# Kernel optimization log

Measured on AMD Instinct MI355X. Metric: run time of the kernel, lower is better.

Reference implementation:

```python
import jax, jax.numpy as jnp
import numpy as np
import math

D_MODEL = 1024
NUM_NEURONS = 2048
LUT_SIZE = 4096
TWO_PI = 2.0 * math.pi


def lut_sin_cos(theta, sin_table, cos_table):
    # Interpolated periodic table lookup over [0, 2*pi)
    n = sin_table.shape[0]
    pos = (theta / TWO_PI) * n
    pos = jnp.mod(pos, n)
    i0 = jnp.floor(pos).astype(jnp.int32)
    frac = pos - i0.astype(theta.dtype)
    i1 = jnp.mod(i0 + 1, n)
    s = sin_table[i0] * (1.0 - frac) + sin_table[i1] * frac
    c = cos_table[i0] * (1.0 - frac) + cos_table[i1] * frac
    return s, c


def setup_inputs() -> dict:
    key = jax.random.key(0)
    ks = jax.random.split(key, 10)
    B = 64
    x_real = jax.random.normal(ks[0], (B, D_MODEL), jnp.float32)
    x_imag = jax.random.normal(ks[1], (B, D_MODEL), jnp.float32)
    t = jax.random.uniform(ks[2], (B,), jnp.float32)
    # xavier_uniform with gain=0.5 for linear weights
    def xavier(k, shape, gain):
        fan_out, fan_in = shape
        a = gain * math.sqrt(6.0 / (fan_in + fan_out))
        return jax.random.uniform(k, shape, jnp.float32, -a, a)
    ic_w = xavier(ks[3], (D_MODEL, 2 * D_MODEL), 0.5)
    ic_b = jnp.zeros((D_MODEL,), jnp.float32)
    W = jax.random.normal(ks[4], (NUM_NEURONS, D_MODEL), jnp.float32) * 0.02
    Bp = jnp.zeros((NUM_NEURONS, D_MODEL), jnp.float32)
    attn_cos = jnp.ones((NUM_NEURONS, D_MODEL), jnp.float32)
    attn_sin = jnp.ones((NUM_NEURONS, D_MODEL), jnp.float32)
    wr = xavier(ks[5], (D_MODEL, NUM_NEURONS), 0.5)
    wi = xavier(ks[6], (D_MODEL, NUM_NEURONS), 0.5)
    grid = jnp.arange(LUT_SIZE, dtype=jnp.float32) * (TWO_PI / LUT_SIZE)
    sin_table = jnp.sin(grid)
    cos_table = jnp.cos(grid)
    return {"x_real": x_real, "x_imag": x_imag, "t": t,
            "ic_w": ic_w, "ic_b": ic_b, "W": W, "Bp": Bp,
            "attn_cos": attn_cos, "attn_sin": attn_sin,
            "wr": wr, "wi": wi,
            "sin_table": sin_table, "cos_table": cos_table}


def reference(x_real, x_imag, t, ic_w, ic_b, W, Bp, attn_cos, attn_sin, wr, wi, sin_table, cos_table):
    x_combined = jnp.concatenate([x_real, x_imag], axis=-1)          # [B, 2D]
    x_collapsed = x_combined @ ic_w.T + ic_b                          # [B, D]
    wavelength = 1.0 + jnp.abs(W)                                     # [N, D]
    theta = x_collapsed[:, None, :] / wavelength + Bp + t[:, None, None]  # [B, N, D]
    sin_t, cos_t = lut_sin_cos(theta, sin_table, cos_table)
    cos_sum = jnp.einsum('bnd,nd->bn', cos_t, attn_cos)               # fused weight+reduce
    sin_sum = jnp.einsum('bnd,nd->bn', sin_t, attn_sin)
    out_real = jax.nn.silu(cos_sum @ wr.T)                            # [B, D]
    out_imag = jax.nn.silu(sin_sum @ wi.T)
    return out_real, out_imag
```

## Files before the change

kernel.cpp:

```cpp
#include <hip/hip_runtime.h>
#include <stdint.h>

#define DM 1024
#define NN 2048
#define BB 64

static constexpr float INV2PI = 0.15915494309189535f;

__device__ __forceinline__ uint32_t bf16r(float x) {
  uint32_t b = __float_as_uint(x);
  b += 0x7fffu + ((b >> 16) & 1u);
  return b >> 16;
}

__global__ __launch_bounds__(256) void k0_prep(
    const float* __restrict__ xr, const float* __restrict__ xi,
    float* __restrict__ xcombP)
{
  __shared__ float tile[64][65];
  int bid = blockIdx.x;
  int t = threadIdx.x;
  int k0 = bid * 64;
  const float* src = (k0 < 1024) ? xr : xi;
  int koff = k0 & 1023;
  int c = t & 63, rl = t >> 6;
#pragma unroll
  for (int i = 0; i < 16; ++i) {
    int b = rl * 16 + i;
    tile[b][c] = src[b * 1024 + koff + c];
  }
  __syncthreads();
  float2* out2 = (float2*)xcombP;
  int bl = t & 63, kp = t >> 6;
#pragma unroll
  for (int i = 0; i < 8; ++i) {
    int kl = (kp * 8 + i) * 2;
    float2 v = make_float2(tile[bl][kl], tile[bl][kl + 1]);
    out2[(size_t)((k0 + kl) >> 1) * 64 + bl] = v;
  }
}

__global__ __launch_bounds__(1024) void k1_collapse(
    const float* __restrict__ xcombP, const float* __restrict__ icw,
    const float* __restrict__ icb, const float* __restrict__ W,
    float* __restrict__ xcq, float* __restrict__ rinv)
{
  __shared__ float part[16][4][64];
  int bid = blockIdx.x;
  int t = threadIdx.x;
  if (bid >= 256) {
    int j = bid - 256;
    const float4* W4 = (const float4*)W;
    float4* R4 = (float4*)rinv;
    int base = j * 2048 + t;
#pragma unroll
    for (int i = 0; i < 2; ++i) {
      int idx = base + i * 1024;
      float4 w = W4[idx];
      float4 r;
      r.x = 1.0f / (1.0f + fabsf(w.x));
      r.y = 1.0f / (1.0f + fabsf(w.y));
      r.z = 1.0f / (1.0f + fabsf(w.z));
      r.w = 1.0f / (1.0f + fabsf(w.w));
      R4[idx] = r;
    }
    return;
  }
  int d0 = bid * 4;
  int wave = __builtin_amdgcn_readfirstlane((int)(t >> 6));
  int lane = t & 63;
  const float2* P2 = (const float2*)xcombP;
  float acc[4] = {0.f, 0.f, 0.f, 0.f};
  int kbase = wave * 128;
  for (int kk = 0; kk < 128; kk += 4) {
    int k = kbase + kk;
    float2 xa = P2[(size_t)(k >> 1) * 64 + lane];
    float2 xb = P2[(size_t)((k >> 1) + 1) * 64 + lane];
#pragma unroll
    for (int r = 0; r < 4; ++r) {
      float4 w = *(const float4*)(icw + (size_t)(d0 + r) * 2048 + k);
      acc[r] = fmaf(w.x, xa.x, acc[r]);
      acc[r] = fmaf(w.y, xa.y, acc[r]);
      acc[r] = fmaf(w.z, xb.x, acc[r]);
      acc[r] = fmaf(w.w, xb.y, acc[r]);
    }
  }
#pragma unroll
  for (int r = 0; r < 4; ++r) part[wave][r][lane] = acc[r];
  __syncthreads();
  if (t < 128) {
    int pj = t >> 6;
    int b = t & 63;
    float s0 = 0.f, s1 = 0.f;
#pragma unroll
    for (int w = 0; w < 16; ++w) {
      s0 += part[w][2 * pj][b];
      s1 += part[w][2 * pj + 1][b];
    }
    float x0 = (s0 + icb[d0 + 2 * pj]) * INV2PI;
    float x1 = (s1 + icb[d0 + 2 * pj + 1]) * INV2PI;
    ((float2*)xcq)[(size_t)bid * 128 + b * 2 + pj] = make_float2(x0, x1);
  }
}

#define K2_STEP(r4, b4, a4, s4, xv)                                       \
  do {                                                                     \
    float rv0 = fmaf((xv).x, (r4).x, fmaf((b4).x, INV2PI, t2));            \
    accc0 = fmaf(__builtin_amdgcn_cosf(rv0), (a4).x, accc0);               \
    accs0 = fmaf(__builtin_amdgcn_sinf(rv0), (s4).x, accs0);               \
    float rv1 = fmaf((xv).y, (r4).y, fmaf((b4).y, INV2PI, t2));            \
    accc1 = fmaf(__builtin_amdgcn_cosf(rv1), (a4).y, accc1);               \
    accs1 = fmaf(__builtin_amdgcn_sinf(rv1), (s4).y, accs1);               \
    float rv2 = fmaf((xv).z, (r4).z, fmaf((b4).z, INV2PI, t2));            \
    accc0 = fmaf(__builtin_amdgcn_cosf(rv2), (a4).z, accc0);               \
    accs0 = fmaf(__builtin_amdgcn_sinf(rv2), (s4).z, accs0);               \
    float rv3 = fmaf((xv).w, (r4).w, fmaf((b4).w, INV2PI, t2));            \
    accc1 = fmaf(__builtin_amdgcn_cosf(rv3), (a4).w, accc1);               \
    accs1 = fmaf(__builtin_amdgcn_sinf(rv3), (s4).w, accs1);               \
  } while (0)

__global__ __launch_bounds__(512) void k2_resonant(
    const float* __restrict__ xcq, const float* __restrict__ rinv,
    const float* __restrict__ Bp, const float* __restrict__ ac,
    const float* __restrict__ as_, const float* __restrict__ tin,
    uint32_t* __restrict__ cssP)
{
  __shared__ __align__(16) float4 xlds[32][64];
  __shared__ __align__(16) float plds[2][8][4][64];
  int wave = __builtin_amdgcn_readfirstlane((int)(threadIdx.x >> 6));
  int lane = threadIdx.x & 63;
  int bid = blockIdx.x;
  int q = bid & 7;
  int n = (bid >> 3) * 8 + wave;
  float t2 = tin[lane] * INV2PI;

  const char* xsrc = (const char*)xcq + (size_t)q * 32768;
  char* xdst = (char*)&xlds[0][0];
#pragma unroll
  for (int r = 0; r < 4; ++r) {
    int j = wave * 4 + r;
    __builtin_amdgcn_global_load_lds(
        (const __attribute__((address_space(1))) void*)(xsrc + j * 1024 + lane * 16),
        (__attribute__((address_space(3))) void*)(xdst + j * 1024), 16, 0, 0);
  }

  int g = lane >> 4;
  const float* ab = (g == 0) ? rinv : (g == 1) ? Bp : (g == 2) ? ac : as_;
  const float* gp = ab + (size_t)n * 1024 + (size_t)q * 128 + (lane & 15) * 4;
#pragma unroll
  for (int c = 0; c < 2; ++c) {
    __builtin_amdgcn_global_load_lds(
        (const __attribute__((address_space(1))) void*)(gp + c * 64),
        (__attribute__((address_space(3))) void*)&plds[c][wave][0][0], 16, 0, 0);
  }

  __syncthreads();

  float accc0 = 0.f, accs0 = 0.f, accc1 = 0.f, accs1 = 0.f;

#pragma unroll
  for (int c = 0; c < 2; ++c) {
    const float4* pr = (const float4*)&plds[c][wave][0][0];
#pragma unroll 4
    for (int i = 0; i < 16; ++i) {
      int ga = c * 16 + i;
      float4 xv = xlds[ga][lane];
      float4 r4 = pr[i];
      float4 b4 = pr[16 + i];
      float4 a4 = pr[32 + i];
      float4 s4 = pr[48 + i];
      K2_STEP(r4, b4, a4, s4, xv);
    }
  }

  size_t o = ((size_t)q * 2048 + n) * 64 + lane;
  cssP[o] = bf16r(accc0 + accc1) | (bf16r(accs0 + accs1) << 16);
}

__global__ __launch_bounds__(256) void k2b_reduce(
    const uint32_t* __restrict__ cssP,
    uint32_t* __restrict__ csB, uint32_t* __restrict__ ssB)
{
  int i = blockIdx.x * 256 + threadIdx.x;
  int np = i >> 6, b = i & 63;
  int n0 = 2 * np;
  float c0 = 0.f, c1 = 0.f, s0 = 0.f, s1 = 0.f;
#pragma unroll
  for (int j = 0; j < 8; ++j) {
    size_t base = ((size_t)j * 2048 + n0) * 64 + b;
    uint32_t u0 = cssP[base];
    uint32_t u1 = cssP[base + 64];
    c0 += __uint_as_float(u0 << 16);
    s0 += __uint_as_float(u0 & 0xffff0000u);
    c1 += __uint_as_float(u1 << 16);
    s1 += __uint_as_float(u1 & 0xffff0000u);
  }
  csB[i] = bf16r(c0) | (bf16r(c1) << 16);
  ssB[i] = bf16r(s0) | (bf16r(s1) << 16);
}

__global__ __launch_bounds__(1024) void k3_out(
    const uint32_t* __restrict__ csB, const uint32_t* __restrict__ ssB,
    const float* __restrict__ wr, const float* __restrict__ wi,
    float* __restrict__ out)
{
  __shared__ float part[16][4][65];
  int bid = blockIdx.x;
  int sel = bid >> 8;
  int d0 = (bid & 255) * 4;
  int wave = __builtin_amdgcn_readfirstlane((int)(threadIdx.x >> 6));
  int lane = threadIdx.x & 63;
  const uint32_t* src2 = sel ? ssB : csB;
  const float* wt = sel ? wi : wr;
  float acc[4] = {0.f, 0.f, 0.f, 0.f};
  int n0 = wave * 128;
  for (int i = 0; i < 32; ++i) {
    int n = n0 + i * 4;
    uint32_t xu0 = src2[(size_t)(n >> 1) * 64 + lane];
    uint32_t xu1 = src2[(size_t)((n >> 1) + 1) * 64 + lane];
    float cv0 = __uint_as_float(xu0 << 16);
    float cv1 = __uint_as_float(xu0 & 0xffff0000u);
    float cv2 = __uint_as_float(xu1 << 16);
    float cv3 = __uint_as_float(xu1 & 0xffff0000u);
#pragma unroll
    for (int r = 0; r < 4; ++r) {
      float4 wv = *(const float4*)(wt + (size_t)(d0 + r) * 2048 + n);
      acc[r] = fmaf(cv0, wv.x, acc[r]);
      acc[r] = fmaf(cv1, wv.y, acc[r]);
      acc[r] = fmaf(cv2, wv.z, acc[r]);
      acc[r] = fmaf(cv3, wv.w, acc[r]);
    }
  }
#pragma unroll
  for (int r = 0; r < 4; ++r) part[wave][r][lane] = acc[r];
  __syncthreads();
  int t = threadIdx.x;
  if (t < 256) {
    int b = t >> 2, j = t & 3;
    float s = 0.f;
#pragma unroll
    for (int w = 0; w < 16; ++w) s += part[w][j][b];
    float y = s / (1.0f + __expf(-s));
    out[(size_t)sel * 65536 + (size_t)b * 1024 + d0 + j] = y;
  }
}

extern "C" void kernel_launch(void* const* d_in, const int* in_sizes, int n_in,
                              void* d_out, int out_size, void* d_ws, size_t ws_size,
                              hipStream_t stream) {
  const float* xr  = (const float*)d_in[0];
  const float* xi  = (const float*)d_in[1];
  const float* t   = (const float*)d_in[2];
  const float* icw = (const float*)d_in[3];
  const float* icb = (const float*)d_in[4];
  const float* W   = (const float*)d_in[5];
  const float* Bp  = (const float*)d_in[6];
  const float* ac  = (const float*)d_in[7];
  const float* as_ = (const float*)d_in[8];
  const float* wr  = (const float*)d_in[9];
  const float* wi  = (const float*)d_in[10];

  float* ws = (float*)d_ws;
  float* rinv    = ws;
  float* xcombP  = ws + 2097152;
  float* xcq     = ws + 2228224;
  uint32_t* cssP = (uint32_t*)(ws + 2293760);
  uint32_t* csB  = (uint32_t*)(ws + 3342336);
  uint32_t* ssB  = (uint32_t*)(ws + 3407872);
  float* out = (float*)d_out;

  k0_prep<<<dim3(32), dim3(256), 0, stream>>>(xr, xi, xcombP);
  k1_collapse<<<dim3(512), dim3(1024), 0, stream>>>(xcombP, icw, icb, W, xcq, rinv);
  k2_resonant<<<dim3(2048), dim3(512), 0, stream>>>(xcq, rinv, Bp, ac, as_, t, cssP);
  k2b_reduce<<<dim3(256), dim3(256), 0, stream>>>(cssP, csB, ssB);
  k3_out<<<dim3(512), dim3(1024), 0, stream>>>(csB, ssB, wr, wi, out);
}
```

Before: 73.34 us.

## Retile resonant kernel to 4 neurons per wave with double-buffered param loads

Each wave now handles 4 neurons over a 64-wide D chunk (16 chunks instead of 8). Per-neuron parameter tiles are double-buffered in LDS with explicit vmcnt waits, so the next tile's load overlaps the sin/cos compute of the current one. The x tile in LDS is reused across 4 neurons, which cuts its staging traffic and halves the grid. In exchange the partial buffer doubles, the reduce kernel sums 16 partials instead of 8, and correctness leans on hand-written waitcnt values.

```diff
diff --git a/kernel.cpp b/kernel.cpp
--- a/kernel.cpp
+++ b/kernel.cpp
@@ -125,20 +125,20 @@
     const float* __restrict__ as_, const float* __restrict__ tin,
     uint32_t* __restrict__ cssP)
 {
-  __shared__ __align__(16) float4 xlds[32][64];
-  __shared__ __align__(16) float plds[2][8][4][64];
+  __shared__ __align__(16) float4 xlds[16][64];
+  __shared__ __align__(16) float plds[2][8][4][16][4];
   int wave = __builtin_amdgcn_readfirstlane((int)(threadIdx.x >> 6));
   int lane = threadIdx.x & 63;
   int bid = blockIdx.x;
-  int q = bid & 7;
-  int n = (bid >> 3) * 8 + wave;
+  int q = bid & 15;
+  int nbase = (bid >> 4) * 32 + wave * 4;
   float t2 = tin[lane] * INV2PI;
 
-  const char* xsrc = (const char*)xcq + (size_t)q * 32768;
+  const char* xsrc = (const char*)xcq + (size_t)q * 16384;
   char* xdst = (char*)&xlds[0][0];
 #pragma unroll
-  for (int r = 0; r < 4; ++r) {
-    int j = wave * 4 + r;
+  for (int r = 0; r < 2; ++r) {
+    int j = wave * 2 + r;
     __builtin_amdgcn_global_load_lds(
         (const __attribute__((address_space(1))) void*)(xsrc + j * 1024 + lane * 16),
         (__attribute__((address_space(3))) void*)(xdst + j * 1024), 16, 0, 0);
@@ -146,35 +146,42 @@
 
   int g = lane >> 4;
   const float* ab = (g == 0) ? rinv : (g == 1) ? Bp : (g == 2) ? ac : as_;
-  const float* gp = ab + (size_t)n * 1024 + (size_t)q * 128 + (lane & 15) * 4;
-#pragma unroll
-  for (int c = 0; c < 2; ++c) {
-    __builtin_amdgcn_global_load_lds(
-        (const __attribute__((address_space(1))) void*)(gp + c * 64),
-        (__attribute__((address_space(3))) void*)&plds[c][wave][0][0], 16, 0, 0);
-  }
-
-  __syncthreads();
-
-  float accc0 = 0.f, accs0 = 0.f, accc1 = 0.f, accs1 = 0.f;
-
-#pragma unroll
-  for (int c = 0; c < 2; ++c) {
-    const float4* pr = (const float4*)&plds[c][wave][0][0];
+  const float* gp0 = ab + (size_t)nbase * 1024 + (size_t)q * 64 + (lane & 15) * 4;
+
+  __builtin_amdgcn_global_load_lds(
+      (const __attribute__((address_space(1))) void*)gp0,
+      (__attribute__((address_space(3))) void*)&plds[0][wave][0][0][0], 16, 0, 0);
+
+  __syncthreads();
+
+#pragma unroll
+  for (int j = 0; j < 4; ++j) {
+    if (j < 3) {
+      __builtin_amdgcn_global_load_lds(
+          (const __attribute__((address_space(1))) void*)(gp0 + (j + 1) * 1024),
+          (__attribute__((address_space(3))) void*)&plds[(j + 1) & 1][wave][0][0][0],
+          16, 0, 0);
+    }
+    if (j == 1 || j == 2) {
+      asm volatile("s_waitcnt vmcnt(2)" ::: "memory");
+    } else if (j == 3) {
+      asm volatile("s_waitcnt vmcnt(1)" ::: "memory");
+    }
+
+    float accc0 = 0.f, accs0 = 0.f, accc1 = 0.f, accs1 = 0.f;
+    const float4* pr = (const float4*)&plds[j & 1][wave][0][0][0];
 #pragma unroll 4
     for (int i = 0; i < 16; ++i) {
-      int ga = c * 16 + i;
-      float4 xv = xlds[ga][lane];
+      float4 xv = xlds[i][lane];
       float4 r4 = pr[i];
       float4 b4 = pr[16 + i];
       float4 a4 = pr[32 + i];
       float4 s4 = pr[48 + i];
       K2_STEP(r4, b4, a4, s4, xv);
     }
-  }
-
-  size_t o = ((size_t)q * 2048 + n) * 64 + lane;
-  cssP[o] = bf16r(accc0 + accc1) | (bf16r(accs0 + accs1) << 16);
+    size_t o = ((size_t)q * 2048 + nbase + j) * 64 + lane;
+    cssP[o] = bf16r(accc0 + accc1) | (bf16r(accs0 + accs1) << 16);
+  }
 }
 
 __global__ __launch_bounds__(256) void k2b_reduce(
@@ -186,7 +193,7 @@
   int n0 = 2 * np;
   float c0 = 0.f, c1 = 0.f, s0 = 0.f, s1 = 0.f;
 #pragma unroll
-  for (int j = 0; j < 8; ++j) {
+  for (int j = 0; j < 16; ++j) {
     size_t base = ((size_t)j * 2048 + n0) * 64 + b;
     uint32_t u0 = cssP[base];
     uint32_t u1 = cssP[base + 64];
@@ -265,13 +272,13 @@
   float* xcombP  = ws + 2097152;
   float* xcq     = ws + 2228224;
   uint32_t* cssP = (uint32_t*)(ws + 2293760);
-  uint32_t* csB  = (uint32_t*)(ws + 3342336);
-  uint32_t* ssB  = (uint32_t*)(ws + 3407872);
+  uint32_t* csB  = (uint32_t*)(ws + 4390912);
+  uint32_t* ssB  = (uint32_t*)(ws + 4456448);
   float* out = (float*)d_out;
 
   k0_prep<<<dim3(32), dim3(256), 0, stream>>>(xr, xi, xcombP);
   k1_collapse<<<dim3(512), dim3(1024), 0, stream>>>(xcombP, icw, icb, W, xcq, rinv);
-  k2_resonant<<<dim3(2048), dim3(512), 0, stream>>>(xcq, rinv, Bp, ac, as_, t, cssP);
+  k2_resonant<<<dim3(1024), dim3(512), 0, stream>>>(xcq, rinv, Bp, ac, as_, t, cssP);
   k2b_reduce<<<dim3(256), dim3(256), 0, stream>>>(cssP, csB, ssB);
   k3_out<<<dim3(512), dim3(1024), 0, stream>>>(csB, ssB, wr, wi, out);
 }
```

After: 76.90 us. 4.8% more time.
